# Kernel tuning notes

Measured on AMD Instinct MI355X. Metric: run time of the kernel, lower is better.

The kernel has to match this reference:

```python
import jax, jax.numpy as jnp
import numpy as np

START, STOP = 3, 4  # tag_to_ix['<START>'], tag_to_ix['<STOP>']
NEG = -10000.0


def _lstm_dir(x, w_ih, w_hh, b_ih, b_hh, h0, c0, reverse):
    # x: [S, E]; PyTorch gate order i, f, g, o
    H2 = h0.shape[0]
    xg = x @ w_ih.T + b_ih + b_hh  # [S, 4*H2] precompute input part

    def step(carry, xt):
        h, c = carry
        g = xt + h @ w_hh.T
        i, f, gg, o = jnp.split(g, 4)
        i, f, o = jax.nn.sigmoid(i), jax.nn.sigmoid(f), jax.nn.sigmoid(o)
        c = f * c + i * jnp.tanh(gg)
        h = o * jnp.tanh(c)
        return (h, c), h

    _, hs = jax.lax.scan(step, (h0, c0), xg, reverse=reverse)
    return hs  # [S, H2]


def setup_inputs() -> dict:
    key = jax.random.key(0)
    ks = jax.random.split(key, 16)
    S, E, H, T = 8192, 768, 1024, 5
    H2 = H // 2
    inp = {
        "embeddings": jax.random.normal(ks[0], (S, E), jnp.float32),
        "w_ih_f": jax.random.normal(ks[1], (4 * H2, E), jnp.float32) * 0.05,
        "w_hh_f": jax.random.normal(ks[2], (4 * H2, H2), jnp.float32) * 0.05,
        "b_ih_f": jax.random.normal(ks[3], (4 * H2,), jnp.float32) * 0.05,
        "b_hh_f": jax.random.normal(ks[4], (4 * H2,), jnp.float32) * 0.05,
        "w_ih_b": jax.random.normal(ks[5], (4 * H2, E), jnp.float32) * 0.05,
        "w_hh_b": jax.random.normal(ks[6], (4 * H2, H2), jnp.float32) * 0.05,
        "b_ih_b": jax.random.normal(ks[7], (4 * H2,), jnp.float32) * 0.05,
        "b_hh_b": jax.random.normal(ks[8], (4 * H2,), jnp.float32) * 0.05,
        "w_tag": jax.random.normal(ks[9], (T, H), jnp.float32) * 0.05,
        "b_tag": jax.random.normal(ks[10], (T,), jnp.float32) * 0.05,
        "h0_f": jax.random.normal(ks[12], (H2,), jnp.float32),
        "c0_f": jnp.zeros((H2,), jnp.float32),
        "h0_b": jax.random.normal(ks[13], (H2,), jnp.float32),
        "c0_b": jnp.zeros((H2,), jnp.float32),
    }
    trans = jax.random.normal(ks[11], (T, T), jnp.float32)
    trans = trans.at[START, :].set(NEG)  # never transition into START
    trans = trans.at[:, STOP].set(NEG)   # never transition out of STOP
    inp["transitions"] = trans
    return inp


def reference(embeddings, w_ih_f, w_hh_f, b_ih_f, b_hh_f,
              w_ih_b, w_hh_b, b_ih_b, b_hh_b,
              w_tag, b_tag, transitions, h0_f, c0_f, h0_b, c0_b):
    # BiLSTM features (batch=1, seq-major as in the torch module)
    h_f = _lstm_dir(embeddings, w_ih_f, w_hh_f, b_ih_f, b_hh_f, h0_f, c0_f, False)
    h_b = _lstm_dir(embeddings, w_ih_b, w_hh_b, b_ih_b, b_hh_b, h0_b, c0_b, True)
    lstm_out = jnp.concatenate([h_f, h_b], axis=-1)      # [S, H]
    feats = lstm_out @ w_tag.T + b_tag                   # [S, T]

    T = feats.shape[1]
    init = jnp.full((T,), NEG, feats.dtype).at[START].set(0.0)

    def vit_step(fv, feat):
        # m[next, prev] = fv[prev] + transitions[next, prev]
        m = fv[None, :] + transitions                     # [T, T]
        bp = jnp.argmax(m, axis=1)                        # [T] backpointers
        return jnp.max(m, axis=1) + feat, bp

    fv, bps = jax.lax.scan(vit_step, init, feats)         # bps: [S, T]
    terminal = fv + transitions[STOP]
    best = jnp.argmax(terminal)
    path_score = terminal[best]

    def back_step(tag, bp):
        return bp[tag], tag

    _, best_path = jax.lax.scan(back_step, best, bps, reverse=True)  # [S]
    return path_score, best_path
```

## Files before the change

kernel.cpp:

```cpp
#include <hip/hip_runtime.h>
#include <hip/hip_bf16.h>
#include <math.h>

#define DEV static __device__ __forceinline__

DEV float rl(float v, int i){ return __uint_as_float(__builtin_amdgcn_readlane(__float_as_uint(v), i)); }

typedef float f32x16 __attribute__((ext_vector_type(16)));

static constexpr size_t OFF_H     = 0;
static constexpr size_t OFF_FEATS = 33554432;
static constexpr size_t OFF_BPS   = OFF_FEATS + 163840;
static constexpr size_t OFF_FC    = OFF_BPS + 163840;
static constexpr size_t OFF_ECH   = OFF_FC + 5120;
static constexpr size_t OFF_EBEST = OFF_ECH + 1024;
static constexpr size_t OFF_HBUF  = OFF_EBEST + 256;

__global__ __launch_bounds__(512,2) void lstm_k(
    const float* __restrict__ emb,
    const float* __restrict__ whhf, const float* __restrict__ whhb,
    const float* __restrict__ wihf, const float* __restrict__ wihb,
    const float* __restrict__ bihf, const float* __restrict__ bhhf,
    const float* __restrict__ bihb, const float* __restrict__ bhhb,
    const float* __restrict__ h0f, const float* __restrict__ c0f,
    const float* __restrict__ h0b, const float* __restrict__ c0b,
    float* __restrict__ H, unsigned long long* __restrict__ hbuf)
{
  const int b  = blockIdx.x;
  const int d  = b >> 5;
  const int k  = b & 31;
  const int tid = threadIdx.x;
  const int w  = tid >> 6;
  const int l  = tid & 63;

  const float* whh = d ? whhb : whhf;
  const float* wih = d ? wihb : wihf;
  const int grow = (l&3)*512 + k*16 + (l>>2);

  const float* pr = whh + (size_t)grow*512 + w*64;
  f32x16 wr0 = *reinterpret_cast<const f32x16*>(pr);
  f32x16 wr1 = *reinterpret_cast<const f32x16*>(pr+16);
  f32x16 wr2 = *reinterpret_cast<const f32x16*>(pr+32);
  f32x16 wr3 = *reinterpret_cast<const f32x16*>(pr+48);
  const float* pi = wih + (size_t)grow*768 + w*96;
  f32x16 wi0 = *reinterpret_cast<const f32x16*>(pi);
  f32x16 wi1 = *reinterpret_cast<const f32x16*>(pi+16);
  f32x16 wi2 = *reinterpret_cast<const f32x16*>(pi+32);
  f32x16 wi3 = *reinterpret_cast<const f32x16*>(pi+48);
  f32x16 wi4 = *reinterpret_cast<const f32x16*>(pi+64);
  f32x16 wi5 = *reinterpret_cast<const f32x16*>(pi+80);
  asm volatile("" : "+v"(wr0)); asm volatile("" : "+v"(wr1));
  asm volatile("" : "+v"(wr2)); asm volatile("" : "+v"(wr3));
  asm volatile("" : "+v"(wi0)); asm volatile("" : "+v"(wi1));
  asm volatile("" : "+v"(wi2)); asm volatile("" : "+v"(wi3));
  asm volatile("" : "+v"(wi4)); asm volatile("" : "+v"(wi5));

  const float bias = (d?bihb:bihf)[grow] + (d?bhhb:bhhf)[grow];

  const float* h0 = d ? h0b : h0f;
  float hv = h0[w*64 + l];
  float c  = (d?c0b:c0f)[k*16 + (l>>2)];

  __shared__ float part[2][8][64];

#define DOT16(X, OFF, W, B0, B1_, B2_, B3_) \
  _Pragma("unroll") for (int i=0;i<16;i+=4){ \
    B0 =fmaf(rl(X,OFF+i+0),W[i+0],B0 ); B1_=fmaf(rl(X,OFF+i+1),W[i+1],B1_); \
    B2_=fmaf(rl(X,OFF+i+2),W[i+2],B2_); B3_=fmaf(rl(X,OFF+i+3),W[i+3],B3_); }

#define EPART(X0,X1,B0,B1_,B2_,B3_) \
  DOT16(X0, 0, wi0, B0,B1_,B2_,B3_) DOT16(X0,16, wi1, B0,B1_,B2_,B3_) \
  DOT16(X0,32, wi2, B0,B1_,B2_,B3_) DOT16(X0,48, wi3, B0,B1_,B2_,B3_) \
  DOT16(X1, 0, wi4, B0,B1_,B2_,B3_) DOT16(X1,16, wi5, B0,B1_,B2_,B3_)

  float acc_e;
  {
    const int tA = d ? 8191 : 0;
    const float* e = emb + (size_t)tA*768 + w*96 + l;
    float x0 = e[0];
    float x1 = (l<32) ? e[64] : 0.f;
    float b0=0.f,b1=0.f,b2=0.f,b3=0.f;
    EPART(x0,x1,b0,b1,b2,b3);
    acc_e = (b0+b1)+(b2+b3);
  }
  float ev0, ev1;
  {
    const int tB = d ? 8190 : 1;
    const float* e = emb + (size_t)tB*768 + w*96 + l;
    ev0 = e[0];
    ev1 = (l<32) ? e[64] : 0.f;
  }

  for (int s=0; s<8192; s++){
    const int t  = d ? (8191-s) : s;
    const int pb = s & 1;
    float a0=acc_e, a1=0.f, a2=0.f, a3=0.f;
    DOT16(hv, 0, wr0, a0,a1,a2,a3)
    DOT16(hv,16, wr1, a0,a1,a2,a3)
    DOT16(hv,32, wr2, a0,a1,a2,a3)
    DOT16(hv,48, wr3, a0,a1,a2,a3)
    part[pb][w][l] = (a0+a1)+(a2+a3);
    __syncthreads();

    if (w==0){
      float r = ((part[pb][0][l]+part[pb][1][l])+(part[pb][2][l]+part[pb][3][l]))
              + ((part[pb][4][l]+part[pb][5][l])+(part[pb][6][l]+part[pb][7][l])) + bias;
      const bool isg = ((l&3)==2);
      float xx = isg ? 2.f*r : r;
      float sg = 1.f/(1.f + expf(-xx));
      float a  = isg ? fmaf(2.f,sg,-1.f) : sg;
      const int lb = l & ~3;
      float ig = __shfl(a, lb);
      float fg = __shfl(a, lb+1);
      float gg = __shfl(a, lb+2);
      float og = __shfl(a, lb+3);
      if ((l&3)==0){
        c = fmaf(fg, c, ig*gg);
        float h = og * tanhf(c);
        const int unit = k*16 + (l>>2);
        unsigned long long pk = ((unsigned long long)(unsigned)(s+1) << 32)
                              | (unsigned long long)__float_as_uint(h);
        __hip_atomic_store(hbuf + (pb<<10) + d*512 + unit, pk,
                           __ATOMIC_RELAXED, __HIP_MEMORY_SCOPE_AGENT);
        H[(size_t)t*1024 + d*512 + unit] = h;
      }
    }

    if (s<8191){
      float nx0=0.f, nx1=0.f;
      if (s<8190){
        const int t2 = d ? (8189-s) : (s+2);
        const float* e = emb + (size_t)t2*768 + w*96 + l;
        nx0 = e[0];
        nx1 = (l<32) ? e[64] : 0.f;
      }
      float b0=0.f,b1=0.f,b2=0.f,b3=0.f;
      EPART(ev0,ev1,b0,b1,b2,b3);
      acc_e = (b0+b1)+(b2+b3);
      ev0=nx0; ev1=nx1;

      const unsigned long long* hp = hbuf + (pb<<10) + d*512 + w*64 + l;
      const unsigned want = (unsigned)(s+1);
      unsigned long long p0 = __hip_atomic_load(hp, __ATOMIC_RELAXED, __HIP_MEMORY_SCOPE_AGENT);
      while ((unsigned)(p0>>32) < want){
        __builtin_amdgcn_s_sleep(1);
        p0 = __hip_atomic_load(hp, __ATOMIC_RELAXED, __HIP_MEMORY_SCOPE_AGENT);
      }
      hv = __uint_as_float((unsigned)p0);
    }
  }
#undef EPART
#undef DOT16
}

__global__ void feats_k(const float* __restrict__ H, const float* __restrict__ wtag,
                        const float* __restrict__ btag, float* __restrict__ feats)
{
  const int r = blockIdx.x*4 + (threadIdx.x>>6);
  const int l = threadIdx.x & 63;
  const float* hrow = H + (size_t)r*1024;
  float hv[16];
  #pragma unroll
  for (int j=0;j<16;j++) hv[j] = hrow[j*64 + l];
  #pragma unroll
  for (int n=0;n<5;n++){
    const float* wrow = wtag + n*1024;
    float acc = 0.f;
    #pragma unroll
    for (int j=0;j<16;j++) acc = fmaf(hv[j], wrow[j*64+l], acc);
    #pragma unroll
    for (int off=32; off; off>>=1) acc += __shfl_xor(acc, off);
    if (l==0) feats[r*5+n] = acc + btag[n];
  }
}

__global__ void vit_fv(const float* __restrict__ feats, const float* __restrict__ trans,
                       int* __restrict__ bps, float* __restrict__ out, int* __restrict__ ebest)
{
  const int l = threadIdx.x & 63;
  const bool active = (l < 25);
  const int n = l/5;
  float tr0=0,tr1=0,tr2=0,tr3=0,tr4=0;
  if (active){ tr0=trans[n*5+0]; tr1=trans[n*5+1]; tr2=trans[n*5+2]; tr3=trans[n*5+3]; tr4=trans[n*5+4]; }
  const float NEG = -10000.0f;
  float fv0=NEG, fv1=NEG, fv2=NEG, fv3=0.f, fv4=NEG;

  float ring[16];
  #pragma unroll
  for (int j=0;j<16;j++) ring[j] = active ? feats[j*5+n] : 0.f;

  for (int tb=0; tb<8192; tb+=16){
    #pragma unroll
    for (int j=0;j<16;j++){
      const int t = tb + j;
      float ft = ring[j];
      float m = fv0 + tr0; int a = 0; float v;
      v = fv1 + tr1; if (v > m){ m=v; a=1; }
      v = fv2 + tr2; if (v > m){ m=v; a=2; }
      v = fv3 + tr3; if (v > m){ m=v; a=3; }
      v = fv4 + tr4; if (v > m){ m=v; a=4; }
      float fnew = m + ft;
      if (active && (l%5)==0) bps[t*5+n] = a;
      fv0 = __shfl(fnew, 0);  fv1 = __shfl(fnew, 5);  fv2 = __shfl(fnew, 10);
      fv3 = __shfl(fnew, 15); fv4 = __shfl(fnew, 20);
      const int tf = t + 16;
      ring[j] = (active && tf < 8192) ? feats[tf*5+n] : 0.f;
    }
  }
  if (l==0){
    float t0=trans[20], t1=trans[21], t2=trans[22], t3=trans[23], t4=trans[24];
    float m = fv0 + t0; int a = 0; float v;
    v = fv1 + t1; if (v > m){ m=v; a=1; }
    v = fv2 + t2; if (v > m){ m=v; a=2; }
    v = fv3 + t3; if (v > m){ m=v; a=3; }
    v = fv4 + t4; if (v > m){ m=v; a=4; }
    out[0] = m;
    ebest[0] = a;
  }
}

__global__ void bt_maps(const int* __restrict__ bps, int* __restrict__ Fc)
{
  __shared__ int sm[160];
  const int c = blockIdx.x, tid = threadIdx.x;
  for (int idx=tid; idx<160; idx+=64) sm[idx] = bps[c*160+idx];
  __syncthreads();
  if (tid<5){
    int cur = tid;
    for (int j=31;j>=0;j--) cur = sm[j*5+cur];
    Fc[c*5+tid] = cur;
  }
}

__global__ void bt_seq(const int* __restrict__ Fc, const int* __restrict__ ebest,
                       int* __restrict__ echunk)
{
  __shared__ int sm[1280];
  const int tid = threadIdx.x;
  for (int idx=tid; idx<1280; idx+=64) sm[idx]=Fc[idx];
  __syncthreads();
  if (tid==0){
    int e = ebest[0];
    for (int c=255;c>=0;c--){ echunk[c]=e; e = sm[c*5+e]; }
  }
}

__global__ void bt_emit(const int* __restrict__ bps, const int* __restrict__ echunk,
                        float* __restrict__ out)
{
  __shared__ int sm[160];
  const int c=blockIdx.x, tid=threadIdx.x;
  for (int idx=tid; idx<160; idx+=64) sm[idx]=bps[c*160+idx];
  __syncthreads();
  if (tid==0){
    int tag = echunk[c];
    out[1 + c*32 + 31] = (float)tag;
    for (int j=31;j>=1;j--){ tag = sm[j*5+tag]; out[1 + c*32 + j-1] = (float)tag; }
  }
}

extern "C" void kernel_launch(void* const* d_in, const int* in_sizes, int n_in,
                              void* d_out, int out_size, void* d_ws, size_t ws_size,
                              hipStream_t stream)
{
  (void)in_sizes; (void)n_in; (void)out_size; (void)ws_size;
  const float* emb  = (const float*)d_in[0];
  const float* wihf = (const float*)d_in[1];
  const float* whhf = (const float*)d_in[2];
  const float* bihf = (const float*)d_in[3];
  const float* bhhf = (const float*)d_in[4];
  const float* wihb = (const float*)d_in[5];
  const float* whhb = (const float*)d_in[6];
  const float* bihb = (const float*)d_in[7];
  const float* bhhb = (const float*)d_in[8];
  const float* wtag = (const float*)d_in[9];
  const float* btag = (const float*)d_in[10];
  const float* h0f  = (const float*)d_in[11];
  const float* c0f  = (const float*)d_in[12];
  const float* h0b  = (const float*)d_in[13];
  const float* c0b  = (const float*)d_in[14];
  const float* trans= (const float*)d_in[15];
  float* out = (float*)d_out;

  char* ws = (char*)d_ws;
  float* H      = (float*)(ws + OFF_H);
  float* feats  = (float*)(ws + OFF_FEATS);
  int*   bps    = (int*)  (ws + OFF_BPS);
  int*   Fc     = (int*)  (ws + OFF_FC);
  int*   echunk = (int*)  (ws + OFF_ECH);
  int*   ebest  = (int*)  (ws + OFF_EBEST);
  unsigned long long* hbuf = (unsigned long long*)(ws + OFF_HBUF);

  hipMemsetAsync(hbuf, 0, 2*1024*8, stream);

  lstm_k<<<64, 512, 0, stream>>>(emb, whhf, whhb, wihf, wihb,
                                 bihf, bhhf, bihb, bhhb,
                                 h0f, c0f, h0b, c0b, H, hbuf);
  feats_k<<<2048, 256, 0, stream>>>(H, wtag, btag, feats);
  vit_fv<<<1, 64, 0, stream>>>(feats, trans, bps, out, ebest);
  bt_maps<<<256, 64, 0, stream>>>(bps, Fc);
  bt_seq<<<1, 64, 0, stream>>>(Fc, ebest, echunk);
  bt_emit<<<256, 64, 0, stream>>>(bps, echunk, out);
}
```

Before: 16.27 ms.

## Precompute LSTM input projection with a tiled GEMM before the recurrence

Adds a tiled SGEMM kernel that computes the input-gate projection for all timesteps and both directions into a workspace buffer. A new recurrent kernel then reads one precomputed value per step instead of doing the embedding dot product inside the serial loop. This removes the input projection work from the latency-critical recurrence, in exchange for an extra launch and a large intermediate buffer. The new path is only taken if the workspace is big enough; otherwise the old fused kernel runs.

```diff
diff --git a/kernel.cpp b/kernel.cpp
--- a/kernel.cpp
+++ b/kernel.cpp
@@ -15,8 +15,171 @@
 static constexpr size_t OFF_ECH   = OFF_FC + 5120;
 static constexpr size_t OFF_EBEST = OFF_ECH + 1024;
 static constexpr size_t OFF_HBUF  = OFF_EBEST + 256;
-
-__global__ __launch_bounds__(512,2) void lstm_k(
+static constexpr size_t OFF_XG    = OFF_HBUF + 16384;
+static constexpr size_t XG_BYTES  = 2ull*8192*2048*4;
+
+__global__ __launch_bounds__(256) void xg_k(const float* __restrict__ emb,
+                                            const float* __restrict__ wihf,
+                                            const float* __restrict__ wihb,
+                                            float* __restrict__ xg)
+{
+  const int tm = blockIdx.x * 128;
+  const int tn = blockIdx.y * 128;
+  const int tid = threadIdx.x;
+  const int ty = tid >> 4, tx = tid & 15;
+  __shared__ float As[16][132], Bs[16][132];
+  float acc[8][8];
+  #pragma unroll
+  for (int i=0;i<8;i++)
+    #pragma unroll
+    for (int j=0;j<8;j++) acc[i][j] = 0.f;
+
+  const int m  = tid & 127;
+  const int n  = tn + m;
+  const float* wih = (n & 2048) ? wihb : wihf;
+  const float* arow = emb + (size_t)(tm+m)*768;
+  const float* brow = wih + (size_t)(n&2047)*768;
+  const int kq = (tid >> 7) << 2;
+
+  for (int k0=0; k0<768; k0+=16){
+    #pragma unroll
+    for (int r=0;r<2;r++){
+      const int kk = kq + r*8;
+      float4 v = *reinterpret_cast<const float4*>(arow + k0 + kk);
+      As[kk+0][m]=v.x; As[kk+1][m]=v.y; As[kk+2][m]=v.z; As[kk+3][m]=v.w;
+      float4 u = *reinterpret_cast<const float4*>(brow + k0 + kk);
+      Bs[kk+0][m]=u.x; Bs[kk+1][m]=u.y; Bs[kk+2][m]=u.z; Bs[kk+3][m]=u.w;
+    }
+    __syncthreads();
+    #pragma unroll
+    for (int k=0;k<16;k++){
+      float4 a0 = *reinterpret_cast<const float4*>(&As[k][ty*8]);
+      float4 a1 = *reinterpret_cast<const float4*>(&As[k][ty*8+4]);
+      float4 b0 = *reinterpret_cast<const float4*>(&Bs[k][tx*8]);
+      float4 b1 = *reinterpret_cast<const float4*>(&Bs[k][tx*8+4]);
+      float af[8] = {a0.x,a0.y,a0.z,a0.w,a1.x,a1.y,a1.z,a1.w};
+      float bf[8] = {b0.x,b0.y,b0.z,b0.w,b1.x,b1.y,b1.z,b1.w};
+      #pragma unroll
+      for (int i=0;i<8;i++)
+        #pragma unroll
+        for (int j=0;j<8;j++) acc[i][j] = fmaf(af[i], bf[j], acc[i][j]);
+    }
+    __syncthreads();
+  }
+
+  const int dd = tn >> 11;
+  const int nb = tn & 2047;
+  float* xgp = xg + (size_t)dd*8192*2048;
+  #pragma unroll
+  for (int i=0;i<8;i++){
+    float* orow = xgp + (size_t)(tm+ty*8+i)*2048 + nb + tx*8;
+    #pragma unroll
+    for (int j=0;j<8;j+=4){
+      float4 st = { acc[i][j], acc[i][j+1], acc[i][j+2], acc[i][j+3] };
+      *reinterpret_cast<float4*>(orow + j) = st;
+    }
+  }
+}
+
+#define DOT16(X, OFF, W, B0, B1_, B2_, B3_) \
+  _Pragma("unroll") for (int i=0;i<16;i+=4){ \
+    B0 =fmaf(rl(X,OFF+i+0),W[i+0],B0 ); B1_=fmaf(rl(X,OFF+i+1),W[i+1],B1_); \
+    B2_=fmaf(rl(X,OFF+i+2),W[i+2],B2_); B3_=fmaf(rl(X,OFF+i+3),W[i+3],B3_); }
+
+__global__ __launch_bounds__(512,2) void lstm_xg(
+    const float* __restrict__ whhf, const float* __restrict__ whhb,
+    const float* __restrict__ bihf, const float* __restrict__ bhhf,
+    const float* __restrict__ bihb, const float* __restrict__ bhhb,
+    const float* __restrict__ h0f, const float* __restrict__ c0f,
+    const float* __restrict__ h0b, const float* __restrict__ c0b,
+    const float* __restrict__ xg,
+    float* __restrict__ H, unsigned long long* __restrict__ hbuf)
+{
+  const int b  = blockIdx.x;
+  const int d  = b >> 5;
+  const int k  = b & 31;
+  const int tid = threadIdx.x;
+  const int w  = tid >> 6;
+  const int l  = tid & 63;
+
+  const float* whh = d ? whhb : whhf;
+  const int grow = (l&3)*512 + k*16 + (l>>2);
+
+  const float* pr = whh + (size_t)grow*512 + w*64;
+  f32x16 wr0 = *reinterpret_cast<const f32x16*>(pr);
+  f32x16 wr1 = *reinterpret_cast<const f32x16*>(pr+16);
+  f32x16 wr2 = *reinterpret_cast<const f32x16*>(pr+32);
+  f32x16 wr3 = *reinterpret_cast<const f32x16*>(pr+48);
+  asm volatile("" : "+v"(wr0)); asm volatile("" : "+v"(wr1));
+  asm volatile("" : "+v"(wr2)); asm volatile("" : "+v"(wr3));
+
+  const float bias = (d?bihb:bihf)[grow] + (d?bhhb:bhhf)[grow];
+  const float* xgp = xg + (size_t)d*8192*2048;
+
+  const float* h0 = d ? h0b : h0f;
+  float hv = h0[w*64 + l];
+  float c  = (d?c0b:c0f)[k*16 + (l>>2)];
+
+  __shared__ float part[2][8][64];
+
+  float xq0 = 0.f, xq1 = 0.f;
+  if (w==0){
+    xq0 = xgp[(size_t)(d?8191:0)*2048 + grow];
+    xq1 = xgp[(size_t)(d?8190:1)*2048 + grow];
+  }
+
+  for (int s=0; s<8192; s++){
+    const int t  = d ? (8191-s) : s;
+    const int pb = s & 1;
+    float a0=0.f, a1=0.f, a2=0.f, a3=0.f;
+    DOT16(hv, 0, wr0, a0,a1,a2,a3)
+    DOT16(hv,16, wr1, a0,a1,a2,a3)
+    DOT16(hv,32, wr2, a0,a1,a2,a3)
+    DOT16(hv,48, wr3, a0,a1,a2,a3)
+    part[pb][w][l] = (a0+a1)+(a2+a3);
+    __syncthreads();
+
+    if (w==0){
+      float r = ((part[pb][0][l]+part[pb][1][l])+(part[pb][2][l]+part[pb][3][l]))
+              + ((part[pb][4][l]+part[pb][5][l])+(part[pb][6][l]+part[pb][7][l]))
+              + bias + xq0;
+      const bool isg = ((l&3)==2);
+      float xx = isg ? 2.f*r : r;
+      float sg = 1.f/(1.f + expf(-xx));
+      float a  = isg ? fmaf(2.f,sg,-1.f) : sg;
+      const int lb = l & ~3;
+      float ig = __shfl(a, lb);
+      float fg = __shfl(a, lb+1);
+      float gg = __shfl(a, lb+2);
+      float og = __shfl(a, lb+3);
+      if ((l&3)==0){
+        c = fmaf(fg, c, ig*gg);
+        float h = og * tanhf(c);
+        const int unit = k*16 + (l>>2);
+        unsigned long long pk = ((unsigned long long)(unsigned)(s+1) << 32)
+                              | (unsigned long long)__float_as_uint(h);
+        __hip_atomic_store(hbuf + (pb<<10) + d*512 + unit, pk,
+                           __ATOMIC_RELAXED, __HIP_MEMORY_SCOPE_AGENT);
+        H[(size_t)t*1024 + d*512 + unit] = h;
+      }
+      xq0 = xq1;
+      if (s<8190) xq1 = xgp[(size_t)(d?(8189-s):(s+2))*2048 + grow];
+    }
+
+    if (s<8191){
+      const unsigned long long* hp = hbuf + (pb<<10) + d*512 + w*64 + l;
+      const unsigned want = (unsigned)(s+1);
+      unsigned long long p0 = __hip_atomic_load(hp, __ATOMIC_RELAXED, __HIP_MEMORY_SCOPE_AGENT);
+      while ((unsigned)(p0>>32) < want){
+        __builtin_amdgcn_s_sleep(1);
+        p0 = __hip_atomic_load(hp, __ATOMIC_RELAXED, __HIP_MEMORY_SCOPE_AGENT);
+      }
+      hv = __uint_as_float((unsigned)p0);
+    }
+  }
+}
+
+__global__ __launch_bounds__(512,2) void lstm_legacy(
     const float* __restrict__ emb,
     const float* __restrict__ whhf, const float* __restrict__ whhb,
     const float* __restrict__ wihf, const float* __restrict__ wihb,
@@ -56,17 +219,11 @@
   asm volatile("" : "+v"(wi4)); asm volatile("" : "+v"(wi5));
 
   const float bias = (d?bihb:bihf)[grow] + (d?bhhb:bhhf)[grow];
-
   const float* h0 = d ? h0b : h0f;
   float hv = h0[w*64 + l];
   float c  = (d?c0b:c0f)[k*16 + (l>>2)];
 
   __shared__ float part[2][8][64];
-
-#define DOT16(X, OFF, W, B0, B1_, B2_, B3_) \
-  _Pragma("unroll") for (int i=0;i<16;i+=4){ \
-    B0 =fmaf(rl(X,OFF+i+0),W[i+0],B0 ); B1_=fmaf(rl(X,OFF+i+1),W[i+1],B1_); \
-    B2_=fmaf(rl(X,OFF+i+2),W[i+2],B2_); B3_=fmaf(rl(X,OFF+i+3),W[i+3],B3_); }
 
 #define EPART(X0,X1,B0,B1_,B2_,B3_) \
   DOT16(X0, 0, wi0, B0,B1_,B2_,B3_) DOT16(X0,16, wi1, B0,B1_,B2_,B3_) \
@@ -150,7 +307,6 @@
     }
   }
 #undef EPART
-#undef DOT16
 }
 
 __global__ void feats_k(const float* __restrict__ H, const float* __restrict__ wtag,
@@ -263,7 +419,7 @@
                               void* d_out, int out_size, void* d_ws, size_t ws_size,
                               hipStream_t stream)
 {
-  (void)in_sizes; (void)n_in; (void)out_size; (void)ws_size;
+  (void)in_sizes; (void)n_in; (void)out_size;
   const float* emb  = (const float*)d_in[0];
   const float* wihf = (const float*)d_in[1];
   const float* whhf = (const float*)d_in[2];
@@ -290,12 +446,20 @@
   int*   echunk = (int*)  (ws + OFF_ECH);
   int*   ebest  = (int*)  (ws + OFF_EBEST);
   unsigned long long* hbuf = (unsigned long long*)(ws + OFF_HBUF);
+  float* xg     = (float*)(ws + OFF_XG);
 
   hipMemsetAsync(hbuf, 0, 2*1024*8, stream);
 
-  lstm_k<<<64, 512, 0, stream>>>(emb, whhf, whhb, wihf, wihb,
-                                 bihf, bhhf, bihb, bhhb,
-                                 h0f, c0f, h0b, c0b, H, hbuf);
+  const bool use_xg = ws_size >= OFF_XG + XG_BYTES;
+  if (use_xg){
+    xg_k<<<dim3(64,32), 256, 0, stream>>>(emb, wihf, wihb, xg);
+    lstm_xg<<<64, 512, 0, stream>>>(whhf, whhb, bihf, bhhf, bihb, bhhb,
+                                    h0f, c0f, h0b, c0b, xg, H, hbuf);
+  } else {
+    lstm_legacy<<<64, 512, 0, stream>>>(emb, whhf, whhb, wihf, wihb,
+                                        bihf, bhhf, bihb, bhhb,
+                                        h0f, c0f, h0b, c0b, H, hbuf);
+  }
   feats_k<<<2048, 256, 0, stream>>>(H, wtag, btag, feats);
   vit_fv<<<1, 64, 0, stream>>>(feats, trans, bps, out, ebest);
   bt_maps<<<256, 64, 0, stream>>>(bps, Fc);
```

Result: faster. 13.83 ms (-15.0%).
